# Kernel optimization log

Measured on AMD Instinct MI355X. Metric: run time of the kernel, lower is better.

Reference implementation:

```python
import jax, jax.numpy as jnp
import numpy as np

N_NODES = 100000
N_EDGES = 600000
IN_C, HID_C, OUT_C = 128, 128, 64


def setup_inputs() -> dict:
    key = jax.random.key(0)
    k1, k2, k3, k4 = jax.random.split(key, 4)
    x = jax.random.normal(k1, (N_NODES, IN_C), dtype=jnp.float32)
    edge_index = jax.random.randint(k2, (2, N_EDGES), 0, N_NODES, dtype=jnp.int64)
    # Glorot-ish init for linear weights
    W1 = jax.random.normal(k3, (IN_C, HID_C), dtype=jnp.float32) / np.sqrt(IN_C)
    b1 = jnp.zeros((HID_C,), dtype=jnp.float32)
    W2 = jax.random.normal(k4, (HID_C, OUT_C), dtype=jnp.float32) / np.sqrt(HID_C)
    b2 = jnp.zeros((OUT_C,), dtype=jnp.float32)
    prelu_a = jnp.full((1,), 0.25, dtype=jnp.float32)  # torch nn.PReLU default
    return {"x": x, "edge_index": edge_index, "W1": W1, "b1": b1,
            "W2": W2, "b2": b2, "prelu_a": prelu_a}


def _gcn_conv(x, src, dst, norm, W, b, num_nodes):
    # PyG GCNConv: h = x W; out[i] = sum_{(j->i)} norm_ji * h[j] + b
    h = x @ W                                   # [N, C_out]
    msg = h[src] * norm[:, None]                # [E', C_out] gather + scale
    out = jax.ops.segment_sum(msg, dst, num_segments=num_nodes)
    return out + b


def reference(x, edge_index, W1, b1, W2, b2, prelu_a):
    n = x.shape[0]
    # add self-loops
    loops = jnp.arange(n, dtype=edge_index.dtype)
    src = jnp.concatenate([edge_index[0], loops])
    dst = jnp.concatenate([edge_index[1], loops])
    # symmetric normalization deg^{-1/2}[src] * deg^{-1/2}[dst]
    deg = jax.ops.segment_sum(jnp.ones_like(dst, dtype=x.dtype), dst, num_segments=n)
    dinv = jnp.where(deg > 0, jax.lax.rsqrt(deg), 0.0)
    norm = dinv[src] * dinv[dst]
    # dropout p=0.0 -> identity
    h = _gcn_conv(x, src, dst, norm, W1, b1, n)
    h = jnp.where(h >= 0, h, prelu_a * h)       # PReLU (single shared parameter)
    out = _gcn_conv(h, src, dst, norm, W2, b2, n)
    return out
```

## Files before the change

kernel.cpp:

```cpp
#include <hip/hip_runtime.h>


typedef __attribute__((ext_vector_type(8))) short bf16x8;
typedef __attribute__((ext_vector_type(4))) float f32x4;

#define CAP 32

__device__ inline unsigned short f2bf(float f) {
    unsigned int b = __float_as_uint(f);
    b += 0x7FFFu + ((b >> 16) & 1u);
    return (unsigned short)(b >> 16);
}
__device__ inline float bflo(unsigned int u) { return __uint_as_float(u << 16); }
__device__ inline float bfhi(unsigned int u) { return __uint_as_float(u & 0xFFFF0000u); }

__device__ inline int clampi(int s, int n) {
    return ((unsigned)s < (unsigned)n) ? s : 0;
}

__device__ inline void acc8m(float* acc, uint4 v, float m) {
    acc[0] += bflo(v.x) * m; acc[1] += bfhi(v.x) * m;
    acc[2] += bflo(v.y) * m; acc[3] += bfhi(v.y) * m;
    acc[4] += bflo(v.z) * m; acc[5] += bfhi(v.z) * m;
    acc[6] += bflo(v.w) * m; acc[7] += bfhi(v.w) * m;
}

__global__ __launch_bounds__(512) void k_pre2(
    const float* __restrict__ W1, const float* __restrict__ W2,
    unsigned short* __restrict__ Wt1, unsigned short* __restrict__ Wt2,
    int* __restrict__ cnt, int n) {
    const int t = blockIdx.x * 512 + threadIdx.x;
    if (t < 128 * 128) {
        int nn = t >> 7, k = t & 127;
        Wt1[t] = f2bf(W1[k * 128 + nn]);
    } else if (t < 128 * 128 + 64 * 128) {
        int j = t - 128 * 128;
        int nn = j >> 7, k = j & 127;
        Wt2[j] = f2bf(W2[k * 64 + nn]);
    }
    const int n4 = n >> 2;
    for (int i = t; i < n4; i += gridDim.x * 512)
        ((int4*)cnt)[i] = make_int4(0, 0, 0, 0);
    if (blockIdx.x == 0 && threadIdx.x < (n & 3)) cnt[n4 * 4 + threadIdx.x] = 0;
}

__global__ __launch_bounds__(512) void k_conv1(
    const float* __restrict__ x, const unsigned short* __restrict__ Wt,
    float* __restrict__ H1f, int n,
    const int* __restrict__ esrc, const int* __restrict__ edst,
    int* __restrict__ cnt, int* __restrict__ bucket, int e, int nfill) {
    constexpr int PITCH = 136;
    __shared__ unsigned short Bs[128 * PITCH];
    const int tid = threadIdx.x;
    const int b = blockIdx.x;

    if ((b & 3) == 3) {
        const int fid = b >> 2;
        const int t = fid * 512 + tid;
        const int e4 = e >> 2;
        const int4* s4 = (const int4*)esrc;
        const int4* d4 = (const int4*)edst;
        for (int i = t; i < e4; i += nfill * 512) {
            int4 s = s4[i], d = d4[i];
            int p0 = atomicAdd(&cnt[d.x], 1);
            int p1 = atomicAdd(&cnt[d.y], 1);
            int p2 = atomicAdd(&cnt[d.z], 1);
            int p3 = atomicAdd(&cnt[d.w], 1);
            if (p0 < CAP) bucket[(size_t)d.x * CAP + p0] = s.x;
            if (p1 < CAP) bucket[(size_t)d.y * CAP + p1] = s.y;
            if (p2 < CAP) bucket[(size_t)d.z * CAP + p2] = s.z;
            if (p3 < CAP) bucket[(size_t)d.w * CAP + p3] = s.w;
        }
        if (fid == 0 && tid < (e & 3)) {
            int i = e4 * 4 + tid;
            int d = edst[i], s = esrc[i];
            int pos = atomicAdd(&cnt[d], 1);
            if (pos < CAP) bucket[(size_t)d * CAP + pos] = s;
        }
        return;
    }

    const int bx = b - (b >> 2);
    for (int q = tid; q < 128 * 16; q += 512) {
        int row = q >> 4, c16 = q & 15;
        *(uint4*)(Bs + row * PITCH + c16 * 8) =
            *(const uint4*)(Wt + row * 128 + c16 * 8);
    }

    const int wave = tid >> 6, lane = tid & 63;
    const int ml = lane & 15;
    const int g = lane >> 4;
    const int stripe = bx * 8 + wave;

    int ra = stripe * 16 + ml;
    if (ra >= n) ra = n - 1;

    bf16x8 af[4];
#pragma unroll
    for (int ks = 0; ks < 4; ++ks) {
        const float* p = x + (size_t)ra * 128 + ks * 32 + g * 8;
        float4 a0 = *(const float4*)p;
        float4 a1 = *(const float4*)(p + 4);
        uint4 pk;
        pk.x = (unsigned)f2bf(a0.x) | ((unsigned)f2bf(a0.y) << 16);
        pk.y = (unsigned)f2bf(a0.z) | ((unsigned)f2bf(a0.w) << 16);
        pk.z = (unsigned)f2bf(a1.x) | ((unsigned)f2bf(a1.y) << 16);
        pk.w = (unsigned)f2bf(a1.z) | ((unsigned)f2bf(a1.w) << 16);
        af[ks] = *(bf16x8*)&pk;
    }

    __syncthreads();

    f32x4 acc[8];
#pragma unroll
    for (int ct = 0; ct < 8; ++ct) acc[ct] = (f32x4){0.f, 0.f, 0.f, 0.f};

#pragma unroll
    for (int ks = 0; ks < 4; ++ks)
#pragma unroll
        for (int ct = 0; ct < 8; ++ct) {
            bf16x8 bb = *(const bf16x8*)(Bs + (size_t)(ct * 16 + ml) * PITCH + ks * 32 + g * 8);
            acc[ct] = __builtin_amdgcn_mfma_f32_16x16x32_bf16(af[ks], bb, acc[ct], 0, 0, 0);
        }

#pragma unroll
    for (int ct = 0; ct < 8; ++ct)
#pragma unroll
        for (int reg = 0; reg < 4; ++reg) {
            int r = stripe * 16 + g * 4 + reg;
            if (r < n) H1f[(size_t)r * 128 + ct * 16 + ml] = acc[ct][reg];
        }
}

__global__ __launch_bounds__(256) void k_scale(
    const float* __restrict__ H1f, const int* __restrict__ cnt,
    unsigned short* __restrict__ h1s, float* __restrict__ dinv, int n) {
    const int tid = threadIdx.x;
    const int node = blockIdx.x * 16 + tid / 16;
    if (node >= n) return;
    const int c0 = (tid & 15) * 8;
    const float di = rsqrtf(1.0f + (float)cnt[node]);
    if ((tid & 15) == 0) dinv[node] = di;
    const float* p = H1f + (size_t)node * 128 + c0;
    float4 a0 = *(const float4*)p;
    float4 a1 = *(const float4*)(p + 4);
    uint4 pk;
    pk.x = (unsigned)f2bf(a0.x * di) | ((unsigned)f2bf(a0.y * di) << 16);
    pk.y = (unsigned)f2bf(a0.z * di) | ((unsigned)f2bf(a0.w * di) << 16);
    pk.z = (unsigned)f2bf(a1.x * di) | ((unsigned)f2bf(a1.y * di) << 16);
    pk.w = (unsigned)f2bf(a1.z * di) | ((unsigned)f2bf(a1.w * di) << 16);
    *(uint4*)(h1s + (size_t)node * 128 + c0) = pk;
}

__global__ __launch_bounds__(512) void k_gather_gemm(
    const unsigned short* __restrict__ Hs,
    const int* __restrict__ cnt, const float* __restrict__ dinv,
    const int* __restrict__ bucket,
    const float* __restrict__ b1, const float* __restrict__ alpha_p,
    const unsigned short* __restrict__ Wt2,
    unsigned short* __restrict__ H2s,
    int n) {
    constexpr int PITCH = 136;
    __shared__ unsigned short As[32 * PITCH];
    __shared__ unsigned short Bs[64 * PITCH];
    const int tid = threadIdx.x;

    for (int q = tid; q < 64 * 16; q += 512) {
        int row = q >> 4, c16 = q & 15;
        *(uint4*)(Bs + row * PITCH + c16 * 8) =
            *(const uint4*)(Wt2 + row * 128 + c16 * 8);
    }

    const int node = blockIdx.x * 32 + tid / 16;
    const int c0 = (tid & 15) * 8;
    const int lr = tid / 16;

    if (node < n) {
        int c = cnt[node];
        const float di = dinv[node];
        if (c > CAP) c = CAP;

        float acc[8];
        {
            uint4 v = *(const uint4*)(Hs + (size_t)node * 128 + c0);
            acc[0] = bflo(v.x); acc[1] = bfhi(v.x);
            acc[2] = bflo(v.y); acc[3] = bfhi(v.y);
            acc[4] = bflo(v.z); acc[5] = bfhi(v.z);
            acc[6] = bflo(v.w); acc[7] = bfhi(v.w);
        }

        if (c > 0) {
            const int* bp = bucket + (size_t)node * CAP;
            int4 i0 = *(const int4*)bp;
            int4 i1 = *(const int4*)(bp + 4);
            int s0 = clampi(i0.x, n);
            int s1 = (1 < c) ? clampi(i0.y, n) : s0;
            int s2 = (2 < c) ? clampi(i0.z, n) : s0;
            int s3 = (3 < c) ? clampi(i0.w, n) : s0;
            int s4 = (4 < c) ? clampi(i1.x, n) : s0;
            int s5 = (5 < c) ? clampi(i1.y, n) : s0;
            int s6 = (6 < c) ? clampi(i1.z, n) : s0;
            int s7 = (7 < c) ? clampi(i1.w, n) : s0;
            uint4 v0 = *(const uint4*)(Hs + (size_t)s0 * 128 + c0);
            uint4 v1 = *(const uint4*)(Hs + (size_t)s1 * 128 + c0);
            uint4 v2 = *(const uint4*)(Hs + (size_t)s2 * 128 + c0);
            uint4 v3 = *(const uint4*)(Hs + (size_t)s3 * 128 + c0);
            uint4 v4 = *(const uint4*)(Hs + (size_t)s4 * 128 + c0);
            uint4 v5 = *(const uint4*)(Hs + (size_t)s5 * 128 + c0);
            uint4 v6 = *(const uint4*)(Hs + (size_t)s6 * 128 + c0);
            uint4 v7 = *(const uint4*)(Hs + (size_t)s7 * 128 + c0);
            acc8m(acc, v0, 1.0f);
            acc8m(acc, v1, (1 < c) ? 1.0f : 0.0f);
            acc8m(acc, v2, (2 < c) ? 1.0f : 0.0f);
            acc8m(acc, v3, (3 < c) ? 1.0f : 0.0f);
            acc8m(acc, v4, (4 < c) ? 1.0f : 0.0f);
            acc8m(acc, v5, (5 < c) ? 1.0f : 0.0f);
            acc8m(acc, v6, (6 < c) ? 1.0f : 0.0f);
            acc8m(acc, v7, (7 < c) ? 1.0f : 0.0f);

            for (int q = 2; q * 4 < c; ++q) {
                int4 idx = *(const int4*)(bp + q * 4);
                int base = q * 4;
                int t0 = clampi(idx.x, n);
                int t1 = (base + 1 < c) ? clampi(idx.y, n) : t0;
                int t2 = (base + 2 < c) ? clampi(idx.z, n) : t0;
                int t3 = (base + 3 < c) ? clampi(idx.w, n) : t0;
                uint4 u0 = *(const uint4*)(Hs + (size_t)t0 * 128 + c0);
                uint4 u1 = *(const uint4*)(Hs + (size_t)t1 * 128 + c0);
                uint4 u2 = *(const uint4*)(Hs + (size_t)t2 * 128 + c0);
                uint4 u3 = *(const uint4*)(Hs + (size_t)t3 * 128 + c0);
                acc8m(acc, u0, 1.0f);
                acc8m(acc, u1, (base + 1 < c) ? 1.0f : 0.0f);
                acc8m(acc, u2, (base + 2 < c) ? 1.0f : 0.0f);
                acc8m(acc, u3, (base + 3 < c) ? 1.0f : 0.0f);
            }
        }

        const float al = alpha_p[0];
        unsigned short o[8];
#pragma unroll
        for (int j = 0; j < 8; ++j) {
            float t = acc[j] * di + b1[c0 + j];
            t = (t >= 0.f) ? t : al * t;
            o[j] = f2bf(t);
        }
        uint4 pk;
        pk.x = (unsigned)o[0] | ((unsigned)o[1] << 16);
        pk.y = (unsigned)o[2] | ((unsigned)o[3] << 16);
        pk.z = (unsigned)o[4] | ((unsigned)o[5] << 16);
        pk.w = (unsigned)o[6] | ((unsigned)o[7] << 16);
        *(uint4*)(As + lr * PITCH + c0) = pk;
    }
    __syncthreads();

    const int wave = tid >> 6, lane = tid & 63;
    const int ml = lane & 15, g = lane >> 4;
    const int stripe = wave >> 2;
    const int ct = wave & 3;

    bf16x8 af[4];
#pragma unroll
    for (int ks = 0; ks < 4; ++ks)
        af[ks] = *(const bf16x8*)(As + (size_t)(stripe * 16 + ml) * PITCH + ks * 32 + g * 8);

    f32x4 acc2 = (f32x4){0.f, 0.f, 0.f, 0.f};
#pragma unroll
    for (int ks = 0; ks < 4; ++ks) {
        bf16x8 bb = *(const bf16x8*)(Bs + (size_t)(ct * 16 + ml) * PITCH + ks * 32 + g * 8);
        acc2 = __builtin_amdgcn_mfma_f32_16x16x32_bf16(af[ks], bb, acc2, 0, 0, 0);
    }

#pragma unroll
    for (int reg = 0; reg < 4; ++reg) {
        int r = blockIdx.x * 32 + stripe * 16 + g * 4 + reg;
        if (r < n)
            H2s[(size_t)r * 64 + ct * 16 + ml] = f2bf(acc2[reg] * dinv[r]);
    }
}

__global__ void k_gather2(const unsigned short* __restrict__ Hs,
                          const int* __restrict__ cnt, const float* __restrict__ dinv,
                          const int* __restrict__ bucket,
                          const float* __restrict__ b, float* __restrict__ out,
                          int n) {
    constexpr int COLS = 64;
    constexpr int NT = COLS / 8;
    constexpr int G = 256 / NT;
    const int tid = threadIdx.x;
    const int node = blockIdx.x * G + tid / NT;
    if (node >= n) return;
    const int c0 = (tid & (NT - 1)) * 8;

    int c = cnt[node];
    const float di = dinv[node];
    if (c > CAP) c = CAP;

    float acc[8];
    {
        uint4 v = *(const uint4*)(Hs + (size_t)node * COLS + c0);
        acc[0] = bflo(v.x); acc[1] = bfhi(v.x);
        acc[2] = bflo(v.y); acc[3] = bfhi(v.y);
        acc[4] = bflo(v.z); acc[5] = bfhi(v.z);
        acc[6] = bflo(v.w); acc[7] = bfhi(v.w);
    }

    if (c > 0) {
        const int* bp = bucket + (size_t)node * CAP;
        int4 i0 = *(const int4*)bp;
        int4 i1 = *(const int4*)(bp + 4);
        int s0 = clampi(i0.x, n);
        int s1 = (1 < c) ? clampi(i0.y, n) : s0;
        int s2 = (2 < c) ? clampi(i0.z, n) : s0;
        int s3 = (3 < c) ? clampi(i0.w, n) : s0;
        int s4 = (4 < c) ? clampi(i1.x, n) : s0;
        int s5 = (5 < c) ? clampi(i1.y, n) : s0;
        int s6 = (6 < c) ? clampi(i1.z, n) : s0;
        int s7 = (7 < c) ? clampi(i1.w, n) : s0;
        uint4 v0 = *(const uint4*)(Hs + (size_t)s0 * COLS + c0);
        uint4 v1 = *(const uint4*)(Hs + (size_t)s1 * COLS + c0);
        uint4 v2 = *(const uint4*)(Hs + (size_t)s2 * COLS + c0);
        uint4 v3 = *(const uint4*)(Hs + (size_t)s3 * COLS + c0);
        uint4 v4 = *(const uint4*)(Hs + (size_t)s4 * COLS + c0);
        uint4 v5 = *(const uint4*)(Hs + (size_t)s5 * COLS + c0);
        uint4 v6 = *(const uint4*)(Hs + (size_t)s6 * COLS + c0);
        uint4 v7 = *(const uint4*)(Hs + (size_t)s7 * COLS + c0);
        acc8m(acc, v0, 1.0f);
        acc8m(acc, v1, (1 < c) ? 1.0f : 0.0f);
        acc8m(acc, v2, (2 < c) ? 1.0f : 0.0f);
        acc8m(acc, v3, (3 < c) ? 1.0f : 0.0f);
        acc8m(acc, v4, (4 < c) ? 1.0f : 0.0f);
        acc8m(acc, v5, (5 < c) ? 1.0f : 0.0f);
        acc8m(acc, v6, (6 < c) ? 1.0f : 0.0f);
        acc8m(acc, v7, (7 < c) ? 1.0f : 0.0f);

        for (int q = 2; q * 4 < c; ++q) {
            int4 idx = *(const int4*)(bp + q * 4);
            int base = q * 4;
            int t0 = clampi(idx.x, n);
            int t1 = (base + 1 < c) ? clampi(idx.y, n) : t0;
            int t2 = (base + 2 < c) ? clampi(idx.z, n) : t0;
            int t3 = (base + 3 < c) ? clampi(idx.w, n) : t0;
            uint4 u0 = *(const uint4*)(Hs + (size_t)t0 * COLS + c0);
            uint4 u1 = *(const uint4*)(Hs + (size_t)t1 * COLS + c0);
            uint4 u2 = *(const uint4*)(Hs + (size_t)t2 * COLS + c0);
            uint4 u3 = *(const uint4*)(Hs + (size_t)t3 * COLS + c0);
            acc8m(acc, u0, 1.0f);
            acc8m(acc, u1, (base + 1 < c) ? 1.0f : 0.0f);
            acc8m(acc, u2, (base + 2 < c) ? 1.0f : 0.0f);
            acc8m(acc, u3, (base + 3 < c) ? 1.0f : 0.0f);
        }
    }

    *(float4*)(out + (size_t)node * COLS + c0) =
        make_float4(acc[0] * di + b[c0 + 0], acc[1] * di + b[c0 + 1],
                    acc[2] * di + b[c0 + 2], acc[3] * di + b[c0 + 3]);
    *(float4*)(out + (size_t)node * COLS + c0 + 4) =
        make_float4(acc[4] * di + b[c0 + 4], acc[5] * di + b[c0 + 5],
                    acc[6] * di + b[c0 + 6], acc[7] * di + b[c0 + 7]);
}

extern "C" void kernel_launch(void* const* d_in, const int* in_sizes, int n_in,
                              void* d_out, int out_size, void* d_ws, size_t ws_size,
                              hipStream_t stream) {
    const float* x  = (const float*)d_in[0];
    const int*   ei = (const int*)d_in[1];
    const float* W1 = (const float*)d_in[2];
    const float* b1 = (const float*)d_in[3];
    const float* W2 = (const float*)d_in[4];
    const float* b2 = (const float*)d_in[5];
    const float* pa = (const float*)d_in[6];
    float* out = (float*)d_out;

    const int n = in_sizes[0] / 128;
    const int e = in_sizes[1] / 2;
    const int* src = ei;
    const int* dst = ei + e;

    float*          H1f = (float*)d_ws;
    unsigned short* h1s = (unsigned short*)(H1f + (size_t)n * 128);
    unsigned short* h2s = h1s + (size_t)n * 128;
    unsigned short* Wt1 = h2s + (size_t)n * 64;
    unsigned short* Wt2 = Wt1 + 128 * 128;
    float* dinv  = (float*)(Wt2 + 64 * 128);
    int*   cnt   = (int*)(dinv + n);
    int*   bucket = cnt + n;

    const int gblk = ((n + 15) / 16 + 7) / 8;
    const int T = (gblk * 4 + 2) / 3;
    const int nfill = T >> 2;

    k_pre2<<<64, 512, 0, stream>>>(W1, W2, Wt1, Wt2, cnt, n);
    k_conv1<<<T, 512, 0, stream>>>(x, Wt1, H1f, n, src, dst, cnt, bucket,
                                   e, nfill);
    k_scale<<<(n + 15) / 16, 256, 0, stream>>>(H1f, cnt, h1s, dinv, n);
    k_gather_gemm<<<(n + 31) / 32, 512, 0, stream>>>(h1s, cnt, dinv, bucket,
                                                     b1, pa, Wt2, h2s, n);
    k_gather2<<<(n + 31) / 32, 256, 0, stream>>>(h2s, cnt, dinv, bucket,
                                                 b2, out, n);
}
```

Measured before the change: 214.7 us.

## Merge count into bucket records, split edge fill, drop scale kernel

Stores each node's in-degree count in slot 0 of its 32-int bucket record, so the count and the first neighbour indices come from one cache line. Edge bucketing is split: about 70% of edges go in a pre-kernel and the rest inside the conv1 GEMM before its sync. Conv1 writes bf16 directly, which removes the fp32 H1 buffer and the k_scale kernel. Normalization moves into the first gather as per-edge dinv[src]*dinv[dst] weights, with a small k_dinv kernel and a memset added. The costs are extra dinv loads per edge and capacity dropping from 32 to 31 neighbours.

```diff
diff --git a/kernel.cpp b/kernel.cpp
--- a/kernel.cpp
+++ b/kernel.cpp
@@ -4,7 +4,7 @@
 typedef __attribute__((ext_vector_type(8))) short bf16x8;
 typedef __attribute__((ext_vector_type(4))) float f32x4;
 
-#define CAP 32
+#define CAPR 31
 
 __device__ inline unsigned short f2bf(float f) {
     unsigned int b = __float_as_uint(f);
@@ -18,17 +18,18 @@
     return ((unsigned)s < (unsigned)n) ? s : 0;
 }
 
-__device__ inline void acc8m(float* acc, uint4 v, float m) {
-    acc[0] += bflo(v.x) * m; acc[1] += bfhi(v.x) * m;
-    acc[2] += bflo(v.y) * m; acc[3] += bfhi(v.y) * m;
-    acc[4] += bflo(v.z) * m; acc[5] += bfhi(v.z) * m;
-    acc[6] += bflo(v.w) * m; acc[7] += bfhi(v.w) * m;
-}
-
-__global__ __launch_bounds__(512) void k_pre2(
+__device__ inline void acc8m(float* acc, uint4 v, float w) {
+    acc[0] += bflo(v.x) * w; acc[1] += bfhi(v.x) * w;
+    acc[2] += bflo(v.y) * w; acc[3] += bfhi(v.y) * w;
+    acc[4] += bflo(v.z) * w; acc[5] += bfhi(v.z) * w;
+    acc[6] += bflo(v.w) * w; acc[7] += bfhi(v.w) * w;
+}
+
+__global__ __launch_bounds__(512) void k_pre(
     const float* __restrict__ W1, const float* __restrict__ W2,
     unsigned short* __restrict__ Wt1, unsigned short* __restrict__ Wt2,
-    int* __restrict__ cnt, int n) {
+    const int* __restrict__ esrc, const int* __restrict__ edst,
+    int* __restrict__ rec, int ea) {
     const int t = blockIdx.x * 512 + threadIdx.x;
     if (t < 128 * 128) {
         int nn = t >> 7, k = t & 127;
@@ -38,49 +39,31 @@
         int nn = j >> 7, k = j & 127;
         Wt2[j] = f2bf(W2[k * 64 + nn]);
     }
-    const int n4 = n >> 2;
-    for (int i = t; i < n4; i += gridDim.x * 512)
-        ((int4*)cnt)[i] = make_int4(0, 0, 0, 0);
-    if (blockIdx.x == 0 && threadIdx.x < (n & 3)) cnt[n4 * 4 + threadIdx.x] = 0;
+    const int4* s4 = (const int4*)esrc;
+    const int4* d4 = (const int4*)edst;
+    const int stride = gridDim.x * 512;
+    for (int i = t; i < (ea >> 2); i += stride) {
+        int4 s = s4[i], d = d4[i];
+        int p0 = atomicAdd(&rec[(size_t)d.x * 32], 1);
+        int p1 = atomicAdd(&rec[(size_t)d.y * 32], 1);
+        int p2 = atomicAdd(&rec[(size_t)d.z * 32], 1);
+        int p3 = atomicAdd(&rec[(size_t)d.w * 32], 1);
+        if (p0 < CAPR) rec[(size_t)d.x * 32 + 1 + p0] = s.x;
+        if (p1 < CAPR) rec[(size_t)d.y * 32 + 1 + p1] = s.y;
+        if (p2 < CAPR) rec[(size_t)d.z * 32 + 1 + p2] = s.z;
+        if (p3 < CAPR) rec[(size_t)d.w * 32 + 1 + p3] = s.w;
+    }
 }
 
 __global__ __launch_bounds__(512) void k_conv1(
     const float* __restrict__ x, const unsigned short* __restrict__ Wt,
-    float* __restrict__ H1f, int n,
+    unsigned short* __restrict__ H, int n,
     const int* __restrict__ esrc, const int* __restrict__ edst,
-    int* __restrict__ cnt, int* __restrict__ bucket, int e, int nfill) {
+    int* __restrict__ rec, int e, int ea) {
     constexpr int PITCH = 136;
     __shared__ unsigned short Bs[128 * PITCH];
     const int tid = threadIdx.x;
-    const int b = blockIdx.x;
-
-    if ((b & 3) == 3) {
-        const int fid = b >> 2;
-        const int t = fid * 512 + tid;
-        const int e4 = e >> 2;
-        const int4* s4 = (const int4*)esrc;
-        const int4* d4 = (const int4*)edst;
-        for (int i = t; i < e4; i += nfill * 512) {
-            int4 s = s4[i], d = d4[i];
-            int p0 = atomicAdd(&cnt[d.x], 1);
-            int p1 = atomicAdd(&cnt[d.y], 1);
-            int p2 = atomicAdd(&cnt[d.z], 1);
-            int p3 = atomicAdd(&cnt[d.w], 1);
-            if (p0 < CAP) bucket[(size_t)d.x * CAP + p0] = s.x;
-            if (p1 < CAP) bucket[(size_t)d.y * CAP + p1] = s.y;
-            if (p2 < CAP) bucket[(size_t)d.z * CAP + p2] = s.z;
-            if (p3 < CAP) bucket[(size_t)d.w * CAP + p3] = s.w;
-        }
-        if (fid == 0 && tid < (e & 3)) {
-            int i = e4 * 4 + tid;
-            int d = edst[i], s = esrc[i];
-            int pos = atomicAdd(&cnt[d], 1);
-            if (pos < CAP) bucket[(size_t)d * CAP + pos] = s;
-        }
-        return;
-    }
-
-    const int bx = b - (b >> 2);
+
     for (int q = tid; q < 128 * 16; q += 512) {
         int row = q >> 4, c16 = q & 15;
         *(uint4*)(Bs + row * PITCH + c16 * 8) =
@@ -90,7 +73,7 @@
     const int wave = tid >> 6, lane = tid & 63;
     const int ml = lane & 15;
     const int g = lane >> 4;
-    const int stripe = bx * 8 + wave;
+    const int stripe = blockIdx.x * 8 + wave;
 
     int ra = stripe * 16 + ml;
     if (ra >= n) ra = n - 1;
@@ -109,6 +92,13 @@
         af[ks] = *(bf16x8*)&pk;
     }
 
+    for (int i = ea + blockIdx.x * 512 + tid; i < e; i += gridDim.x * 512) {
+        int d = edst[i];
+        int s = esrc[i];
+        int pos = atomicAdd(&rec[(size_t)d * 32], 1);
+        if (pos < CAPR) rec[(size_t)d * 32 + 1 + pos] = s;
+    }
+
     __syncthreads();
 
     f32x4 acc[8];
@@ -128,34 +118,19 @@
 #pragma unroll
         for (int reg = 0; reg < 4; ++reg) {
             int r = stripe * 16 + g * 4 + reg;
-            if (r < n) H1f[(size_t)r * 128 + ct * 16 + ml] = acc[ct][reg];
-        }
-}
-
-__global__ __launch_bounds__(256) void k_scale(
-    const float* __restrict__ H1f, const int* __restrict__ cnt,
-    unsigned short* __restrict__ h1s, float* __restrict__ dinv, int n) {
-    const int tid = threadIdx.x;
-    const int node = blockIdx.x * 16 + tid / 16;
-    if (node >= n) return;
-    const int c0 = (tid & 15) * 8;
-    const float di = rsqrtf(1.0f + (float)cnt[node]);
-    if ((tid & 15) == 0) dinv[node] = di;
-    const float* p = H1f + (size_t)node * 128 + c0;
-    float4 a0 = *(const float4*)p;
-    float4 a1 = *(const float4*)(p + 4);
-    uint4 pk;
-    pk.x = (unsigned)f2bf(a0.x * di) | ((unsigned)f2bf(a0.y * di) << 16);
-    pk.y = (unsigned)f2bf(a0.z * di) | ((unsigned)f2bf(a0.w * di) << 16);
-    pk.z = (unsigned)f2bf(a1.x * di) | ((unsigned)f2bf(a1.y * di) << 16);
-    pk.w = (unsigned)f2bf(a1.z * di) | ((unsigned)f2bf(a1.w * di) << 16);
-    *(uint4*)(h1s + (size_t)node * 128 + c0) = pk;
+            if (r < n) H[(size_t)r * 128 + ct * 16 + ml] = f2bf(acc[ct][reg]);
+        }
+}
+
+__global__ void k_dinv(const int* __restrict__ rec, float* __restrict__ dinv,
+                       int n) {
+    int i = blockIdx.x * 256 + threadIdx.x;
+    if (i < n) dinv[i] = rsqrtf(1.0f + (float)rec[(size_t)i * 32]);
 }
 
 __global__ __launch_bounds__(512) void k_gather_gemm(
-    const unsigned short* __restrict__ Hs,
-    const int* __restrict__ cnt, const float* __restrict__ dinv,
-    const int* __restrict__ bucket,
+    const unsigned short* __restrict__ H,
+    const int* __restrict__ rec, const float* __restrict__ dinv,
     const float* __restrict__ b1, const float* __restrict__ alpha_p,
     const unsigned short* __restrict__ Wt2,
     unsigned short* __restrict__ H2s,
@@ -176,63 +151,70 @@
     const int lr = tid / 16;
 
     if (node < n) {
-        int c = cnt[node];
+        const int* rp = rec + (size_t)node * 32;
+        int4 i0 = *(const int4*)rp;
+        int4 i1 = *(const int4*)(rp + 4);
+        int c = i0.x;
+        if (c > CAPR) c = CAPR;
         const float di = dinv[node];
-        if (c > CAP) c = CAP;
 
         float acc[8];
         {
-            uint4 v = *(const uint4*)(Hs + (size_t)node * 128 + c0);
-            acc[0] = bflo(v.x); acc[1] = bfhi(v.x);
-            acc[2] = bflo(v.y); acc[3] = bfhi(v.y);
-            acc[4] = bflo(v.z); acc[5] = bfhi(v.z);
-            acc[6] = bflo(v.w); acc[7] = bfhi(v.w);
+            uint4 v = *(const uint4*)(H + (size_t)node * 128 + c0);
+            float sl = di * di;
+            acc[0] = bflo(v.x) * sl + b1[c0 + 0];
+            acc[1] = bfhi(v.x) * sl + b1[c0 + 1];
+            acc[2] = bflo(v.y) * sl + b1[c0 + 2];
+            acc[3] = bfhi(v.y) * sl + b1[c0 + 3];
+            acc[4] = bflo(v.z) * sl + b1[c0 + 4];
+            acc[5] = bfhi(v.z) * sl + b1[c0 + 5];
+            acc[6] = bflo(v.w) * sl + b1[c0 + 6];
+            acc[7] = bfhi(v.w) * sl + b1[c0 + 7];
         }
 
         if (c > 0) {
-            const int* bp = bucket + (size_t)node * CAP;
-            int4 i0 = *(const int4*)bp;
-            int4 i1 = *(const int4*)(bp + 4);
-            int s0 = clampi(i0.x, n);
-            int s1 = (1 < c) ? clampi(i0.y, n) : s0;
-            int s2 = (2 < c) ? clampi(i0.z, n) : s0;
-            int s3 = (3 < c) ? clampi(i0.w, n) : s0;
-            int s4 = (4 < c) ? clampi(i1.x, n) : s0;
-            int s5 = (5 < c) ? clampi(i1.y, n) : s0;
-            int s6 = (6 < c) ? clampi(i1.z, n) : s0;
-            int s7 = (7 < c) ? clampi(i1.w, n) : s0;
-            uint4 v0 = *(const uint4*)(Hs + (size_t)s0 * 128 + c0);
-            uint4 v1 = *(const uint4*)(Hs + (size_t)s1 * 128 + c0);
-            uint4 v2 = *(const uint4*)(Hs + (size_t)s2 * 128 + c0);
-            uint4 v3 = *(const uint4*)(Hs + (size_t)s3 * 128 + c0);
-            uint4 v4 = *(const uint4*)(Hs + (size_t)s4 * 128 + c0);
-            uint4 v5 = *(const uint4*)(Hs + (size_t)s5 * 128 + c0);
-            uint4 v6 = *(const uint4*)(Hs + (size_t)s6 * 128 + c0);
-            uint4 v7 = *(const uint4*)(Hs + (size_t)s7 * 128 + c0);
-            acc8m(acc, v0, 1.0f);
-            acc8m(acc, v1, (1 < c) ? 1.0f : 0.0f);
-            acc8m(acc, v2, (2 < c) ? 1.0f : 0.0f);
-            acc8m(acc, v3, (3 < c) ? 1.0f : 0.0f);
-            acc8m(acc, v4, (4 < c) ? 1.0f : 0.0f);
-            acc8m(acc, v5, (5 < c) ? 1.0f : 0.0f);
-            acc8m(acc, v6, (6 < c) ? 1.0f : 0.0f);
-            acc8m(acc, v7, (7 < c) ? 1.0f : 0.0f);
-
-            for (int q = 2; q * 4 < c; ++q) {
-                int4 idx = *(const int4*)(bp + q * 4);
-                int base = q * 4;
+            int s1 = clampi(i0.y, n);
+            int s2 = (2 <= c) ? clampi(i0.z, n) : s1;
+            int s3 = (3 <= c) ? clampi(i0.w, n) : s1;
+            int s4 = (4 <= c) ? clampi(i1.x, n) : s1;
+            int s5 = (5 <= c) ? clampi(i1.y, n) : s1;
+            int s6 = (6 <= c) ? clampi(i1.z, n) : s1;
+            int s7 = (7 <= c) ? clampi(i1.w, n) : s1;
+            uint4 v1 = *(const uint4*)(H + (size_t)s1 * 128 + c0);
+            uint4 v2 = *(const uint4*)(H + (size_t)s2 * 128 + c0);
+            uint4 v3 = *(const uint4*)(H + (size_t)s3 * 128 + c0);
+            uint4 v4 = *(const uint4*)(H + (size_t)s4 * 128 + c0);
+            uint4 v5 = *(const uint4*)(H + (size_t)s5 * 128 + c0);
+            uint4 v6 = *(const uint4*)(H + (size_t)s6 * 128 + c0);
+            uint4 v7 = *(const uint4*)(H + (size_t)s7 * 128 + c0);
+            float w1 = dinv[s1] * di;
+            float w2 = (2 <= c) ? dinv[s2] * di : 0.0f;
+            float w3 = (3 <= c) ? dinv[s3] * di : 0.0f;
+            float w4 = (4 <= c) ? dinv[s4] * di : 0.0f;
+            float w5 = (5 <= c) ? dinv[s5] * di : 0.0f;
+            float w6 = (6 <= c) ? dinv[s6] * di : 0.0f;
+            float w7 = (7 <= c) ? dinv[s7] * di : 0.0f;
+            acc8m(acc, v1, w1); acc8m(acc, v2, w2);
+            acc8m(acc, v3, w3); acc8m(acc, v4, w4);
+            acc8m(acc, v5, w5); acc8m(acc, v6, w6);
+            acc8m(acc, v7, w7);
+
+            for (int base = 8; base <= c; base += 4) {
+                int4 idx = *(const int4*)(rp + base);
                 int t0 = clampi(idx.x, n);
-                int t1 = (base + 1 < c) ? clampi(idx.y, n) : t0;
-                int t2 = (base + 2 < c) ? clampi(idx.z, n) : t0;
-                int t3 = (base + 3 < c) ? clampi(idx.w, n) : t0;
-                uint4 u0 = *(const uint4*)(Hs + (size_t)t0 * 128 + c0);
-                uint4 u1 = *(const uint4*)(Hs + (size_t)t1 * 128 + c0);
-                uint4 u2 = *(const uint4*)(Hs + (size_t)t2 * 128 + c0);
-                uint4 u3 = *(const uint4*)(Hs + (size_t)t3 * 128 + c0);
-                acc8m(acc, u0, 1.0f);
-                acc8m(acc, u1, (base + 1 < c) ? 1.0f : 0.0f);
-                acc8m(acc, u2, (base + 2 < c) ? 1.0f : 0.0f);
-                acc8m(acc, u3, (base + 3 < c) ? 1.0f : 0.0f);
+                int t1 = (base + 1 <= c) ? clampi(idx.y, n) : t0;
+                int t2 = (base + 2 <= c) ? clampi(idx.z, n) : t0;
+                int t3 = (base + 3 <= c) ? clampi(idx.w, n) : t0;
+                uint4 u0 = *(const uint4*)(H + (size_t)t0 * 128 + c0);
+                uint4 u1 = *(const uint4*)(H + (size_t)t1 * 128 + c0);
+                uint4 u2 = *(const uint4*)(H + (size_t)t2 * 128 + c0);
+                uint4 u3 = *(const uint4*)(H + (size_t)t3 * 128 + c0);
+                float y0 = dinv[t0] * di;
+                float y1 = (base + 1 <= c) ? dinv[t1] * di : 0.0f;
+                float y2 = (base + 2 <= c) ? dinv[t2] * di : 0.0f;
+                float y3 = (base + 3 <= c) ? dinv[t3] * di : 0.0f;
+                acc8m(acc, u0, y0); acc8m(acc, u1, y1);
+                acc8m(acc, u2, y2); acc8m(acc, u3, y3);
             }
         }
 
@@ -240,7 +222,7 @@
         unsigned short o[8];
 #pragma unroll
         for (int j = 0; j < 8; ++j) {
-            float t = acc[j] * di + b1[c0 + j];
+            float t = acc[j];
             t = (t >= 0.f) ? t : al * t;
             o[j] = f2bf(t);
         }
@@ -279,8 +261,7 @@
 }
 
 __global__ void k_gather2(const unsigned short* __restrict__ Hs,
-                          const int* __restrict__ cnt, const float* __restrict__ dinv,
-                          const int* __restrict__ bucket,
+                          const int* __restrict__ rec, const float* __restrict__ dinv,
                           const float* __restrict__ b, float* __restrict__ out,
                           int n) {
     constexpr int COLS = 64;
@@ -291,9 +272,12 @@
     if (node >= n) return;
     const int c0 = (tid & (NT - 1)) * 8;
 
-    int c = cnt[node];
+    const int* rp = rec + (size_t)node * 32;
+    int4 i0 = *(const int4*)rp;
+    int4 i1 = *(const int4*)(rp + 4);
+    int c = i0.x;
+    if (c > CAPR) c = CAPR;
     const float di = dinv[node];
-    if (c > CAP) c = CAP;
 
     float acc[8];
     {
@@ -305,18 +289,13 @@
     }
 
     if (c > 0) {
-        const int* bp = bucket + (size_t)node * CAP;
-        int4 i0 = *(const int4*)bp;
-        int4 i1 = *(const int4*)(bp + 4);
-        int s0 = clampi(i0.x, n);
-        int s1 = (1 < c) ? clampi(i0.y, n) : s0;
-        int s2 = (2 < c) ? clampi(i0.z, n) : s0;
-        int s3 = (3 < c) ? clampi(i0.w, n) : s0;
-        int s4 = (4 < c) ? clampi(i1.x, n) : s0;
-        int s5 = (5 < c) ? clampi(i1.y, n) : s0;
-        int s6 = (6 < c) ? clampi(i1.z, n) : s0;
-        int s7 = (7 < c) ? clampi(i1.w, n) : s0;
-        uint4 v0 = *(const uint4*)(Hs + (size_t)s0 * COLS + c0);
+        int s1 = clampi(i0.y, n);
+        int s2 = (2 <= c) ? clampi(i0.z, n) : s1;
+        int s3 = (3 <= c) ? clampi(i0.w, n) : s1;
+        int s4 = (4 <= c) ? clampi(i1.x, n) : s1;
+        int s5 = (5 <= c) ? clampi(i1.y, n) : s1;
+        int s6 = (6 <= c) ? clampi(i1.z, n) : s1;
+        int s7 = (7 <= c) ? clampi(i1.w, n) : s1;
         uint4 v1 = *(const uint4*)(Hs + (size_t)s1 * COLS + c0);
         uint4 v2 = *(const uint4*)(Hs + (size_t)s2 * COLS + c0);
         uint4 v3 = *(const uint4*)(Hs + (size_t)s3 * COLS + c0);
@@ -324,30 +303,28 @@
         uint4 v5 = *(const uint4*)(Hs + (size_t)s5 * COLS + c0);
         uint4 v6 = *(const uint4*)(Hs + (size_t)s6 * COLS + c0);
         uint4 v7 = *(const uint4*)(Hs + (size_t)s7 * COLS + c0);
-        acc8m(acc, v0, 1.0f);
-        acc8m(acc, v1, (1 < c) ? 1.0f : 0.0f);
-        acc8m(acc, v2, (2 < c) ? 1.0f : 0.0f);
-        acc8m(acc, v3, (3 < c) ? 1.0f : 0.0f);
-        acc8m(acc, v4, (4 < c) ? 1.0f : 0.0f);
-        acc8m(acc, v5, (5 < c) ? 1.0f : 0.0f);
-        acc8m(acc, v6, (6 < c) ? 1.0f : 0.0f);
-        acc8m(acc, v7, (7 < c) ? 1.0f : 0.0f);
-
-        for (int q = 2; q * 4 < c; ++q) {
-            int4 idx = *(const int4*)(bp + q * 4);
-            int base = q * 4;
+        acc8m(acc, v1, 1.0f);
+        acc8m(acc, v2, (2 <= c) ? 1.0f : 0.0f);
+        acc8m(acc, v3, (3 <= c) ? 1.0f : 0.0f);
+        acc8m(acc, v4, (4 <= c) ? 1.0f : 0.0f);
+        acc8m(acc, v5, (5 <= c) ? 1.0f : 0.0f);
+        acc8m(acc, v6, (6 <= c) ? 1.0f : 0.0f);
+        acc8m(acc, v7, (7 <= c) ? 1.0f : 0.0f);
+
+        for (int base = 8; base <= c; base += 4) {
+            int4 idx = *(const int4*)(rp + base);
             int t0 = clampi(idx.x, n);
-            int t1 = (base + 1 < c) ? clampi(idx.y, n) : t0;
-            int t2 = (base + 2 < c) ? clampi(idx.z, n) : t0;
-            int t3 = (base + 3 < c) ? clampi(idx.w, n) : t0;
+            int t1 = (base + 1 <= c) ? clampi(idx.y, n) : t0;
+            int t2 = (base + 2 <= c) ? clampi(idx.z, n) : t0;
+            int t3 = (base + 3 <= c) ? clampi(idx.w, n) : t0;
             uint4 u0 = *(const uint4*)(Hs + (size_t)t0 * COLS + c0);
             uint4 u1 = *(const uint4*)(Hs + (size_t)t1 * COLS + c0);
             uint4 u2 = *(const uint4*)(Hs + (size_t)t2 * COLS + c0);
             uint4 u3 = *(const uint4*)(Hs + (size_t)t3 * COLS + c0);
             acc8m(acc, u0, 1.0f);
-            acc8m(acc, u1, (base + 1 < c) ? 1.0f : 0.0f);
-            acc8m(acc, u2, (base + 2 < c) ? 1.0f : 0.0f);
-            acc8m(acc, u3, (base + 3 < c) ? 1.0f : 0.0f);
+            acc8m(acc, u1, (base + 1 <= c) ? 1.0f : 0.0f);
+            acc8m(acc, u2, (base + 2 <= c) ? 1.0f : 0.0f);
+            acc8m(acc, u3, (base + 3 <= c) ? 1.0f : 0.0f);
         }
     }
 
@@ -376,25 +353,25 @@
     const int* src = ei;
     const int* dst = ei + e;
 
-    float*          H1f = (float*)d_ws;
-    unsigned short* h1s = (unsigned short*)(H1f + (size_t)n * 128);
-    unsigned short* h2s = h1s + (size_t)n * 128;
+    unsigned short* h1  = (unsigned short*)d_ws;
+    unsigned short* h2s = h1 + (size_t)n * 128;
     unsigned short* Wt1 = h2s + (size_t)n * 64;
     unsigned short* Wt2 = Wt1 + 128 * 128;
-    float* dinv  = (float*)(Wt2 + 64 * 128);
-    int*   cnt   = (int*)(dinv + n);
-    int*   bucket = cnt + n;
+    float* dinv = (float*)(Wt2 + 64 * 128);
+    int*   rec  = (int*)(dinv + n);
+
+    int EA = (int)(((long long)e * 7) / 10) & ~3;
+    if ((e & 3) != 0) EA = 0;
 
     const int gblk = ((n + 15) / 16 + 7) / 8;
-    const int T = (gblk * 4 + 2) / 3;
-    const int nfill = T >> 2;
-
-    k_pre2<<<64, 512, 0, stream>>>(W1, W2, Wt1, Wt2, cnt, n);
-    k_conv1<<<T, 512, 0, stream>>>(x, Wt1, H1f, n, src, dst, cnt, bucket,
-                                   e, nfill);
-    k_scale<<<(n + 15) / 16, 256, 0, stream>>>(H1f, cnt, h1s, dinv, n);
-    k_gather_gemm<<<(n + 31) / 32, 512, 0, stream>>>(h1s, cnt, dinv, bucket,
-                                                     b1, pa, Wt2, h2s, n);
-    k_gather2<<<(n + 31) / 32, 256, 0, stream>>>(h2s, cnt, dinv, bucket,
-                                                 b2, out, n);
-}
+    int pblk = (EA / 4 + 511) / 512;
+    if (pblk < 48) pblk = 48;
+
+    hipMemsetAsync(rec, 0, (size_t)n * 32 * sizeof(int), stream);
+    k_pre<<<pblk, 512, 0, stream>>>(W1, W2, Wt1, Wt2, src, dst, rec, EA);
+    k_conv1<<<gblk, 512, 0, stream>>>(x, Wt1, h1, n, src, dst, rec, e, EA);
+    k_dinv<<<(n + 255) / 256, 256, 0, stream>>>(rec, dinv, n);
+    k_gather_gemm<<<(n + 31) / 32, 512, 0, stream>>>(h1, rec, dinv, b1, pa,
+                                                     Wt2, h2s, n);
+    k_gather2<<<(n + 31) / 32, 256, 0, stream>>>(h2s, rec, dinv, b2, out, n);
+}
```

Result: faster. 205.8 us (-4.1%).
